# Kernel tuning notes

Hardware: AMD Instinct MI355X
Metric: run time of the kernel (lower is better)

Reference implementation:

```python
import jax, jax.numpy as jnp
import numpy as np

B, M, N, DQ, H = 4, 4096, 4096, 256, 64

def setup_inputs() -> dict:
    key = jax.random.key(0)
    k1, k2, k3, k4 = jax.random.split(key, 4)
    x = jax.random.normal(k1, (B, M, DQ), dtype=jnp.float32)
    cond = jax.random.normal(k2, (B, N, DQ), dtype=jnp.float32)
    Wq = jax.random.normal(k3, (DQ, H), dtype=jnp.float32) * (1.0 / np.sqrt(DQ))
    Wkv = jax.random.normal(k4, (DQ, 2 * H), dtype=jnp.float32) * (1.0 / np.sqrt(DQ))
    return {"x": x, "cond": cond, "Wq": Wq, "Wkv": Wkv}

def reference(x, cond, Wq, Wkv):
    h = Wq.shape[1]
    q = jnp.einsum('bmi,ih->bmh', x, Wq)          # [B,M,H]
    kv = jnp.einsum('bni,ih->bnh', cond, Wkv)     # [B,N,2H]
    k, v = jnp.split(kv, 2, axis=-1)              # each [B,N,H]
    qk = jnp.einsum('bmd,bnd->bmn', q, k) / jnp.sqrt(jnp.asarray(h, q.dtype))
    attn = jax.nn.softmax(qk, axis=-1)            # [B,M,N]
    out = jnp.einsum('bmn,bnd->bmd', attn, v)     # [B,M,H]
    return out
```

## Files before the change

### kernel.cpp

```cpp
#include <hip/hip_runtime.h>
#include <hip/hip_bf16.h>
#include <cstdint>


#define BB 4
#define MM 4096
#define NN 4096
#define DQm 256
#define DH 64
#define NSP 8
#define NITER (NN / 64 / NSP)
#define QSCALE 0.18033688011112042f

typedef _Float16 half8 __attribute__((ext_vector_type(8)));
typedef _Float16 half4 __attribute__((ext_vector_type(4)));
typedef float floatx16 __attribute__((ext_vector_type(16)));

static __device__ __forceinline__ unsigned pkrtz(float a, float b) {
    union { __fp16 h __attribute__((ext_vector_type(2))); unsigned u; } cv;
    cv.h = __builtin_amdgcn_cvt_pkrtz(a, b);
    return cv.u;
}

__global__ __launch_bounds__(256) void wtrans_kernel(const float* __restrict__ Wq,
                                                     const float* __restrict__ Wkv,
                                                     _Float16* __restrict__ wt) {
    int cout = blockIdx.x;
    int t = threadIdx.x;
    float v = (cout < 64) ? Wq[t * 64 + cout] * QSCALE : Wkv[t * 128 + (cout - 64)];
    _Float16 hi = (_Float16)v;
    _Float16 lo = (_Float16)(v - (float)hi);
    wt[cout * DQm + t] = hi;
    wt[192 * DQm + cout * DQm + t] = lo;
}

__global__ __launch_bounds__(256) void proj_kernel(const float* __restrict__ x,
                                                   const float* __restrict__ cond,
                                                   const _Float16* __restrict__ wt,
                                                   _Float16* __restrict__ q_h,
                                                   _Float16* __restrict__ k_h,
                                                   _Float16* __restrict__ vt_h) {
    __shared__ __align__(16) _Float16 xh[64][264];
    __shared__ __align__(16) _Float16 xl[64][264];
    const int t = threadIdx.x;
    const bool isq = blockIdx.x < (BB * MM / 64);
    const int blk = isq ? blockIdx.x : blockIdx.x - BB * MM / 64;
    const long row0 = (long)blk * 64;
    const float4* xg = (const float4*)((isq ? x : cond) + row0 * DQm);
#pragma unroll
    for (int it = 0; it < 16; ++it) {
        int fid = t + it * 256;
        int row = fid >> 6, c4 = fid & 63;
        float4 v = xg[fid];
        half4 hh = {(_Float16)v.x, (_Float16)v.y, (_Float16)v.z, (_Float16)v.w};
        half4 hl = {(_Float16)(v.x - (float)hh[0]), (_Float16)(v.y - (float)hh[1]),
                    (_Float16)(v.z - (float)hh[2]), (_Float16)(v.w - (float)hh[3])};
        *(half4*)(&xh[row][c4 * 4]) = hh;
        *(half4*)(&xl[row][c4 * 4]) = hl;
    }
    __syncthreads();
    const int lane = t & 63, w = t >> 6, c = lane & 31, h = lane >> 5;
    const _Float16* wlo = wt + 192 * DQm;

    if (isq) {
        const int rt = w & 1, ct = w >> 1;
        floatx16 a1, a2, a3;
#pragma unroll
        for (int i = 0; i < 16; ++i) { a1[i] = 0.f; a2[i] = 0.f; a3[i] = 0.f; }
#pragma unroll
        for (int kt = 0; kt < 16; ++kt) {
            half8 ah = *(const half8*)(&xh[rt * 32 + c][kt * 16 + h * 8]);
            half8 al = *(const half8*)(&xl[rt * 32 + c][kt * 16 + h * 8]);
            half8 bh = *(const half8*)(wt  + (long)(ct * 32 + c) * DQm + kt * 16 + h * 8);
            half8 bl = *(const half8*)(wlo + (long)(ct * 32 + c) * DQm + kt * 16 + h * 8);
            a1 = __builtin_amdgcn_mfma_f32_32x32x16_f16(ah, bh, a1, 0, 0, 0);
            a2 = __builtin_amdgcn_mfma_f32_32x32x16_f16(ah, bl, a2, 0, 0, 0);
            a3 = __builtin_amdgcn_mfma_f32_32x32x16_f16(al, bh, a3, 0, 0, 0);
        }
#pragma unroll
        for (int r = 0; r < 16; ++r) {
            int m = (r & 3) + 8 * (r >> 2) + 4 * h;
            q_h[(row0 + rt * 32 + m) * DH + ct * 32 + c] = (_Float16)(a1[r] + a2[r] + a3[r]);
        }
    } else {
        const int rt = w & 1, ctp = w >> 1;
        floatx16 a1[2], a2[2], a3[2];
#pragma unroll
        for (int i = 0; i < 16; ++i) {
            a1[0][i] = 0.f; a2[0][i] = 0.f; a3[0][i] = 0.f;
            a1[1][i] = 0.f; a2[1][i] = 0.f; a3[1][i] = 0.f;
        }
#pragma unroll
        for (int kt = 0; kt < 16; ++kt) {
            half8 ah = *(const half8*)(&xh[rt * 32 + c][kt * 16 + h * 8]);
            half8 al = *(const half8*)(&xl[rt * 32 + c][kt * 16 + h * 8]);
#pragma unroll
            for (int i = 0; i < 2; ++i) {
                long wrow = 64 + (ctp * 2 + i) * 32 + c;
                half8 bh = *(const half8*)(wt  + wrow * DQm + kt * 16 + h * 8);
                half8 bl = *(const half8*)(wlo + wrow * DQm + kt * 16 + h * 8);
                a1[i] = __builtin_amdgcn_mfma_f32_32x32x16_f16(ah, bh, a1[i], 0, 0, 0);
                a2[i] = __builtin_amdgcn_mfma_f32_32x32x16_f16(ah, bl, a2[i], 0, 0, 0);
                a3[i] = __builtin_amdgcn_mfma_f32_32x32x16_f16(al, bh, a3[i], 0, 0, 0);
            }
        }
#pragma unroll
        for (int i = 0; i < 2; ++i) {
            int cout = (ctp * 2 + i) * 32 + c;
            if (cout < 64) {
#pragma unroll
                for (int r = 0; r < 16; ++r) {
                    int m = (r & 3) + 8 * (r >> 2) + 4 * h;
                    k_h[(row0 + rt * 32 + m) * DH + cout] =
                        (_Float16)(a1[i][r] + a2[i][r] + a3[i][r]);
                }
            } else {
                int d = cout - 64;
                long bb = row0 >> 12;
#pragma unroll
                for (int s2 = 0; s2 < 4; ++s2) {
                    long n = row0 + rt * 32 + 8 * s2 + 4 * h;
                    half4 hv;
#pragma unroll
                    for (int j = 0; j < 4; ++j)
                        hv[j] = (_Float16)(a1[i][s2 * 4 + j] + a2[i][s2 * 4 + j] +
                                           a3[i][s2 * 4 + j]);
                    *(half4*)(vt_h + (bb * DH + d) * NN + (n & 4095)) = hv;
                }
            }
        }
    }
}

__global__ __launch_bounds__(256, 4) void fa_kernel(const _Float16* __restrict__ q_h,
                                                    const _Float16* __restrict__ k_h,
                                                    const _Float16* __restrict__ vt_h,
                                                    float* __restrict__ Opart,
                                                    float2* __restrict__ ml) {
    __shared__ __align__(16) _Float16 k_lds[64][72];
    __shared__ __align__(16) _Float16 vt_lds[64][72];

    const int t = threadIdx.x;
    const int w = t >> 6;
    const int lane = t & 63;
    const int c = lane & 31;
    const int h = lane >> 5;

    const int bid = blockIdx.x;
    const int sp = bid >> 7;
    const int b  = (bid >> 5) & 3;
    const int mt = bid & 31;
    const int mbase = mt * 128 + w * 32;
    const long qrow = (long)b * MM + mbase + c;

    half8 qf[4];
#pragma unroll
    for (int kt = 0; kt < 4; ++kt)
        qf[kt] = *(const half8*)(q_h + qrow * DH + kt * 16 + h * 8);

    floatx16 Oc0, Oc1;
#pragma unroll
    for (int i = 0; i < 16; ++i) { Oc0[i] = 0.f; Oc1[i] = 0.f; }
    float m_run = -INFINITY, l_run = 0.f;

#pragma unroll 1
    for (int nt = sp * NITER; nt < sp * NITER + NITER; ++nt) {
        const int n0 = nt * 64;
        __syncthreads();
        {
            const uint4* kg = (const uint4*)(k_h + ((long)b * NN + n0) * DH);
#pragma unroll
            for (int it = 0; it < 2; ++it) {
                int cid = t + it * 256;
                int r = cid >> 3, q = cid & 7;
                *(uint4*)(&k_lds[r][q * 8]) = kg[cid];
                *(uint4*)(&vt_lds[r][q * 8]) =
                    *(const uint4*)(vt_h + ((long)b * DH + r) * NN + n0 + q * 8);
            }
        }
        __syncthreads();

        floatx16 Sc[2];
#pragma unroll
        for (int a = 0; a < 2; ++a) {
            floatx16 acc;
#pragma unroll
            for (int i = 0; i < 16; ++i) acc[i] = 0.f;
#pragma unroll
            for (int kt = 0; kt < 4; ++kt) {
                half8 af = *(const half8*)(&k_lds[a * 32 + c][kt * 16 + h * 8]);
                acc = __builtin_amdgcn_mfma_f32_32x32x16_f16(af, qf[kt], acc, 0, 0, 0);
            }
            Sc[a] = acc;
        }

        float tmax = -INFINITY;
#pragma unroll
        for (int a = 0; a < 2; ++a)
#pragma unroll
            for (int r = 0; r < 16; ++r) tmax = fmaxf(tmax, Sc[a][r]);
        tmax = fmaxf(tmax, __shfl_xor(tmax, 32, 64));
        if (__any(tmax > m_run + 8.0f)) {
            float m_new = fmaxf(m_run, tmax);
            float alpha = exp2f(m_run - m_new);
            l_run *= alpha;
#pragma unroll
            for (int i = 0; i < 16; ++i) { Oc0[i] *= alpha; Oc1[i] *= alpha; }
            m_run = m_new;
        }
        float tsum = 0.f;
#pragma unroll
        for (int a = 0; a < 2; ++a)
#pragma unroll
            for (int r = 0; r < 16; ++r) {
                float p = exp2f(Sc[a][r] - m_run);
                Sc[a][r] = p;
                tsum += p;
            }
        tsum += __shfl_xor(tsum, 32, 64);
        l_run += tsum;

#pragma unroll
        for (int a = 0; a < 2; ++a) {
            uint2 pk0 = {pkrtz(Sc[a][0],  Sc[a][1]),  pkrtz(Sc[a][2],  Sc[a][3])};
            uint2 pk1 = {pkrtz(Sc[a][4],  Sc[a][5]),  pkrtz(Sc[a][6],  Sc[a][7])};
            uint2 pk2 = {pkrtz(Sc[a][8],  Sc[a][9]),  pkrtz(Sc[a][10], Sc[a][11])};
            uint2 pk3 = {pkrtz(Sc[a][12], Sc[a][13]), pkrtz(Sc[a][14], Sc[a][15])};
            union { uint4 u; half8 f; } f0, f1;
#if __has_builtin(__builtin_amdgcn_permlane32_swap)
            {
                auto r0 = __builtin_amdgcn_permlane32_swap(pk0.x, pk1.x, false, false);
                auto r1 = __builtin_amdgcn_permlane32_swap(pk0.y, pk1.y, false, false);
                auto r2 = __builtin_amdgcn_permlane32_swap(pk2.x, pk3.x, false, false);
                auto r3 = __builtin_amdgcn_permlane32_swap(pk2.y, pk3.y, false, false);
                f0.u.x = r0[0]; f0.u.z = r0[1];
                f0.u.y = r1[0]; f0.u.w = r1[1];
                f1.u.x = r2[0]; f1.u.z = r2[1];
                f1.u.y = r3[0]; f1.u.w = r3[1];
            }
#else
            {
                uint2 s0, s1, ex0, ex1;
                s0.x = h ? pk0.x : pk1.x;  s0.y = h ? pk0.y : pk1.y;
                s1.x = h ? pk2.x : pk3.x;  s1.y = h ? pk2.y : pk3.y;
                ex0.x = __shfl_xor((int)s0.x, 32, 64);
                ex0.y = __shfl_xor((int)s0.y, 32, 64);
                ex1.x = __shfl_xor((int)s1.x, 32, 64);
                ex1.y = __shfl_xor((int)s1.y, 32, 64);
                f0.u.x = h ? ex0.x : pk0.x;  f0.u.y = h ? ex0.y : pk0.y;
                f0.u.z = h ? pk1.x : ex0.x;  f0.u.w = h ? pk1.y : ex0.y;
                f1.u.x = h ? ex1.x : pk2.x;  f1.u.y = h ? ex1.y : pk2.y;
                f1.u.z = h ? pk3.x : ex1.x;  f1.u.w = h ? pk3.y : ex1.y;
            }
#endif
#pragma unroll
            for (int bq = 0; bq < 2; ++bq) {
                int kt = 2 * a + bq;
                half8 pf = bq ? f1.f : f0.f;
                half8 vf0 = *(const half8*)(&vt_lds[c][kt * 16 + h * 8]);
                half8 vf1 = *(const half8*)(&vt_lds[32 + c][kt * 16 + h * 8]);
                Oc0 = __builtin_amdgcn_mfma_f32_32x32x16_f16(vf0, pf, Oc0, 0, 0, 0);
                Oc1 = __builtin_amdgcn_mfma_f32_32x32x16_f16(vf1, pf, Oc1, 0, 0, 0);
            }
        }
    }

    const long obase = ((long)sp * BB * MM + (long)b * MM + mbase + c) * DH;
#pragma unroll
    for (int dt = 0; dt < 2; ++dt) {
        const floatx16& O = dt ? Oc1 : Oc0;
#pragma unroll
        for (int s2 = 0; s2 < 4; ++s2) {
            float4 v;
            v.x = O[s2 * 4 + 0]; v.y = O[s2 * 4 + 1];
            v.z = O[s2 * 4 + 2]; v.w = O[s2 * 4 + 3];
            *(float4*)(Opart + obase + dt * 32 + s2 * 8 + h * 4) = v;
        }
    }
    if (h == 0)
        ml[((long)sp * BB + b) * MM + mbase + c] = make_float2(m_run, l_run);
}

__global__ __launch_bounds__(256) void merge_kernel(const float* __restrict__ Opart,
                                                    const float2* __restrict__ ml,
                                                    float* __restrict__ out) {
    const long gid = (long)blockIdx.x * 256 + threadIdx.x;
    const long row = gid >> 6;
    float2 p[NSP];
    float mmax = -INFINITY;
#pragma unroll
    for (int i = 0; i < NSP; ++i) {
        p[i] = ml[(long)i * BB * MM + row];
        mmax = fmaxf(mmax, p[i].x);
    }
    float denom = 0.f, o = 0.f;
#pragma unroll
    for (int i = 0; i < NSP; ++i) {
        float ai = exp2f(p[i].x - mmax);
        denom += ai * p[i].y;
        o += ai * Opart[(long)i * BB * MM * DH + gid];
    }
    out[gid] = o / denom;
}

extern "C" void kernel_launch(void* const* d_in, const int* in_sizes, int n_in,
                              void* d_out, int out_size, void* d_ws, size_t ws_size,
                              hipStream_t stream) {
    const float* x    = (const float*)d_in[0];
    const float* cond = (const float*)d_in[1];
    const float* Wq   = (const float*)d_in[2];
    const float* Wkv  = (const float*)d_in[3];
    float* out = (float*)d_out;

    char* ws = (char*)d_ws;
    _Float16* wt   = (_Float16*)(ws);
    _Float16* q_h  = (_Float16*)(ws + 196608);
    _Float16* k_h  = (_Float16*)(ws + 196608 + 2097152);
    _Float16* vt_h = (_Float16*)(ws + 196608 + 2 * 2097152);
    float*    Op   = (float*)(ws + 196608 + 3 * 2097152);
    float2*   mlp  = (float2*)(ws + 196608 + 3 * 2097152 + (size_t)NSP * 4194304);

    wtrans_kernel<<<192, 256, 0, stream>>>(Wq, Wkv, wt);
    proj_kernel<<<BB * (MM + NN) / 64, 256, 0, stream>>>(x, cond, wt, q_h, k_h, vt_h);
    fa_kernel<<<NSP * BB * 32, 256, 0, stream>>>(q_h, k_h, vt_h, Op, mlp);
    merge_kernel<<<BB * MM * DH / 256, 256, 0, stream>>>(Op, mlp, out);
}
```

Baseline: 134.9 us.

## Double-buffer K/V tiles, compute row sums via MFMA, vectorize merge

The flash-attention loop now keeps two LDS buffers. It prefetches the next K/V tile into registers while the current tile is computed, and needs only one barrier per iteration instead of two. Row sums of P are computed by an extra MFMA against a ones fragment instead of a VALU reduction with a cross-lane shuffle, and the tile max uses a tree reduction. The merge kernel handles four outputs per thread with float4 loads and stores. The cost is doubled LDS, extra prefetch registers that may hurt occupancy at 4 waves per SIMD, and an additional MFMA per P-V step.

```diff
diff --git a/kernel.cpp b/kernel.cpp
--- a/kernel.cpp
+++ b/kernel.cpp
@@ -137,8 +137,8 @@
                                                     const _Float16* __restrict__ vt_h,
                                                     float* __restrict__ Opart,
                                                     float2* __restrict__ ml) {
-    __shared__ __align__(16) _Float16 k_lds[64][72];
-    __shared__ __align__(16) _Float16 vt_lds[64][72];
+    __shared__ __align__(16) _Float16 k_lds[2][64][72];
+    __shared__ __align__(16) _Float16 vt_lds[2][64][72];
 
     const int t = threadIdx.x;
     const int w = t >> 6;
@@ -153,32 +153,52 @@
     const int mbase = mt * 128 + w * 32;
     const long qrow = (long)b * MM + mbase + c;
 
+    const int r0 = t >> 3, qq = t & 7;
+    const uint4* kg = (const uint4*)(k_h + (long)b * NN * DH);
+    const _Float16* vp0 = vt_h + ((long)b * DH + r0) * NN + qq * 8;
+    const _Float16* vp1 = vp0 + 32 * NN;
+
     half8 qf[4];
 #pragma unroll
     for (int kt = 0; kt < 4; ++kt)
         qf[kt] = *(const half8*)(q_h + qrow * DH + kt * 16 + h * 8);
 
-    floatx16 Oc0, Oc1;
-#pragma unroll
-    for (int i = 0; i < 16; ++i) { Oc0[i] = 0.f; Oc1[i] = 0.f; }
-    float m_run = -INFINITY, l_run = 0.f;
+    half8 ones_frag;
+    {
+        const _Float16 ov = (c == 0 || c == 4) ? (_Float16)1.0f : (_Float16)0.0f;
+#pragma unroll
+        for (int j = 0; j < 8; ++j) ones_frag[j] = ov;
+    }
+
+    floatx16 Oc0, Oc1, Lc;
+#pragma unroll
+    for (int i = 0; i < 16; ++i) { Oc0[i] = 0.f; Oc1[i] = 0.f; Lc[i] = 0.f; }
+    float m_run = -INFINITY;
+
+    uint4 sk0, sk1, sv0, sv1;
+    {
+        const int n0 = sp * NITER * 64;
+        sk0 = kg[n0 * 8 + t];
+        sk1 = kg[n0 * 8 + t + 256];
+        sv0 = *(const uint4*)(vp0 + n0);
+        sv1 = *(const uint4*)(vp1 + n0);
+        *(uint4*)(&k_lds[0][r0][qq * 8]) = sk0;
+        *(uint4*)(&k_lds[0][r0 + 32][qq * 8]) = sk1;
+        *(uint4*)(&vt_lds[0][r0][qq * 8]) = sv0;
+        *(uint4*)(&vt_lds[0][r0 + 32][qq * 8]) = sv1;
+    }
+    __syncthreads();
 
 #pragma unroll 1
-    for (int nt = sp * NITER; nt < sp * NITER + NITER; ++nt) {
-        const int n0 = nt * 64;
-        __syncthreads();
-        {
-            const uint4* kg = (const uint4*)(k_h + ((long)b * NN + n0) * DH);
-#pragma unroll
-            for (int it = 0; it < 2; ++it) {
-                int cid = t + it * 256;
-                int r = cid >> 3, q = cid & 7;
-                *(uint4*)(&k_lds[r][q * 8]) = kg[cid];
-                *(uint4*)(&vt_lds[r][q * 8]) =
-                    *(const uint4*)(vt_h + ((long)b * DH + r) * NN + n0 + q * 8);
-            }
-        }
-        __syncthreads();
+    for (int it = 0; it < NITER; ++it) {
+        const int pb = it & 1;
+        if (it + 1 < NITER) {
+            const int n0 = (sp * NITER + it + 1) * 64;
+            sk0 = kg[n0 * 8 + t];
+            sk1 = kg[n0 * 8 + t + 256];
+            sv0 = *(const uint4*)(vp0 + n0);
+            sv1 = *(const uint4*)(vp1 + n0);
+        }
 
         floatx16 Sc[2];
 #pragma unroll
@@ -188,37 +208,33 @@
             for (int i = 0; i < 16; ++i) acc[i] = 0.f;
 #pragma unroll
             for (int kt = 0; kt < 4; ++kt) {
-                half8 af = *(const half8*)(&k_lds[a * 32 + c][kt * 16 + h * 8]);
+                half8 af = *(const half8*)(&k_lds[pb][a * 32 + c][kt * 16 + h * 8]);
                 acc = __builtin_amdgcn_mfma_f32_32x32x16_f16(af, qf[kt], acc, 0, 0, 0);
             }
             Sc[a] = acc;
         }
 
-        float tmax = -INFINITY;
-#pragma unroll
-        for (int a = 0; a < 2; ++a)
-#pragma unroll
-            for (int r = 0; r < 16; ++r) tmax = fmaxf(tmax, Sc[a][r]);
+        float t8[8];
+#pragma unroll
+        for (int i = 0; i < 8; ++i)
+            t8[i] = fmaxf(fmaxf(Sc[0][2 * i], Sc[0][2 * i + 1]),
+                          fmaxf(Sc[1][2 * i], Sc[1][2 * i + 1]));
+        float ta = fmaxf(fmaxf(t8[0], t8[1]), t8[2]);
+        float tb = fmaxf(fmaxf(t8[3], t8[4]), t8[5]);
+        float tmax = fmaxf(fmaxf(ta, tb), fmaxf(t8[6], t8[7]));
         tmax = fmaxf(tmax, __shfl_xor(tmax, 32, 64));
         if (__any(tmax > m_run + 8.0f)) {
             float m_new = fmaxf(m_run, tmax);
             float alpha = exp2f(m_run - m_new);
-            l_run *= alpha;
 #pragma unroll
             for (int i = 0; i < 16; ++i) { Oc0[i] *= alpha; Oc1[i] *= alpha; }
+            Lc[0] *= alpha;
             m_run = m_new;
         }
-        float tsum = 0.f;
 #pragma unroll
         for (int a = 0; a < 2; ++a)
 #pragma unroll
-            for (int r = 0; r < 16; ++r) {
-                float p = exp2f(Sc[a][r] - m_run);
-                Sc[a][r] = p;
-                tsum += p;
-            }
-        tsum += __shfl_xor(tsum, 32, 64);
-        l_run += tsum;
+            for (int r = 0; r < 16; ++r) Sc[a][r] = exp2f(Sc[a][r] - m_run);
 
 #pragma unroll
         for (int a = 0; a < 2; ++a) {
@@ -229,14 +245,14 @@
             union { uint4 u; half8 f; } f0, f1;
 #if __has_builtin(__builtin_amdgcn_permlane32_swap)
             {
-                auto r0 = __builtin_amdgcn_permlane32_swap(pk0.x, pk1.x, false, false);
-                auto r1 = __builtin_amdgcn_permlane32_swap(pk0.y, pk1.y, false, false);
-                auto r2 = __builtin_amdgcn_permlane32_swap(pk2.x, pk3.x, false, false);
-                auto r3 = __builtin_amdgcn_permlane32_swap(pk2.y, pk3.y, false, false);
-                f0.u.x = r0[0]; f0.u.z = r0[1];
-                f0.u.y = r1[0]; f0.u.w = r1[1];
-                f1.u.x = r2[0]; f1.u.z = r2[1];
-                f1.u.y = r3[0]; f1.u.w = r3[1];
+                auto r0s = __builtin_amdgcn_permlane32_swap(pk0.x, pk1.x, false, false);
+                auto r1s = __builtin_amdgcn_permlane32_swap(pk0.y, pk1.y, false, false);
+                auto r2s = __builtin_amdgcn_permlane32_swap(pk2.x, pk3.x, false, false);
+                auto r3s = __builtin_amdgcn_permlane32_swap(pk2.y, pk3.y, false, false);
+                f0.u.x = r0s[0]; f0.u.z = r0s[1];
+                f0.u.y = r1s[0]; f0.u.w = r1s[1];
+                f1.u.x = r2s[0]; f1.u.z = r2s[1];
+                f1.u.y = r3s[0]; f1.u.w = r3s[1];
             }
 #else
             {
@@ -257,11 +273,21 @@
             for (int bq = 0; bq < 2; ++bq) {
                 int kt = 2 * a + bq;
                 half8 pf = bq ? f1.f : f0.f;
-                half8 vf0 = *(const half8*)(&vt_lds[c][kt * 16 + h * 8]);
-                half8 vf1 = *(const half8*)(&vt_lds[32 + c][kt * 16 + h * 8]);
+                half8 vf0 = *(const half8*)(&vt_lds[pb][c][kt * 16 + h * 8]);
+                half8 vf1 = *(const half8*)(&vt_lds[pb][32 + c][kt * 16 + h * 8]);
                 Oc0 = __builtin_amdgcn_mfma_f32_32x32x16_f16(vf0, pf, Oc0, 0, 0, 0);
                 Oc1 = __builtin_amdgcn_mfma_f32_32x32x16_f16(vf1, pf, Oc1, 0, 0, 0);
-            }
+                Lc  = __builtin_amdgcn_mfma_f32_32x32x16_f16(ones_frag, pf, Lc, 0, 0, 0);
+            }
+        }
+
+        if (it + 1 < NITER) {
+            const int pn = pb ^ 1;
+            *(uint4*)(&k_lds[pn][r0][qq * 8]) = sk0;
+            *(uint4*)(&k_lds[pn][r0 + 32][qq * 8]) = sk1;
+            *(uint4*)(&vt_lds[pn][r0][qq * 8]) = sv0;
+            *(uint4*)(&vt_lds[pn][r0 + 32][qq * 8]) = sv1;
+            __syncthreads();
         }
     }
 
@@ -278,14 +304,14 @@
         }
     }
     if (h == 0)
-        ml[((long)sp * BB + b) * MM + mbase + c] = make_float2(m_run, l_run);
+        ml[((long)sp * BB + b) * MM + mbase + c] = make_float2(m_run, Lc[0]);
 }
 
 __global__ __launch_bounds__(256) void merge_kernel(const float* __restrict__ Opart,
                                                     const float2* __restrict__ ml,
                                                     float* __restrict__ out) {
-    const long gid = (long)blockIdx.x * 256 + threadIdx.x;
-    const long row = gid >> 6;
+    const long g4 = (long)blockIdx.x * 256 + threadIdx.x;
+    const long row = g4 >> 4;
     float2 p[NSP];
     float mmax = -INFINITY;
 #pragma unroll
@@ -293,14 +319,19 @@
         p[i] = ml[(long)i * BB * MM + row];
         mmax = fmaxf(mmax, p[i].x);
     }
-    float denom = 0.f, o = 0.f;
+    float denom = 0.f;
+    float4 o = make_float4(0.f, 0.f, 0.f, 0.f);
+    const float4* Op4 = (const float4*)Opart;
 #pragma unroll
     for (int i = 0; i < NSP; ++i) {
         float ai = exp2f(p[i].x - mmax);
         denom += ai * p[i].y;
-        o += ai * Opart[(long)i * BB * MM * DH + gid];
-    }
-    out[gid] = o / denom;
+        float4 v = Op4[(long)i * (BB * MM * DH / 4) + g4];
+        o.x += ai * v.x; o.y += ai * v.y; o.z += ai * v.z; o.w += ai * v.w;
+    }
+    float inv = 1.0f / denom;
+    o.x *= inv; o.y *= inv; o.z *= inv; o.w *= inv;
+    ((float4*)out)[g4] = o;
 }
 
 extern "C" void kernel_launch(void* const* d_in, const int* in_sizes, int n_in,
@@ -323,5 +354,5 @@
     wtrans_kernel<<<192, 256, 0, stream>>>(Wq, Wkv, wt);
     proj_kernel<<<BB * (MM + NN) / 64, 256, 0, stream>>>(x, cond, wt, q_h, k_h, vt_h);
     fa_kernel<<<NSP * BB * 32, 256, 0, stream>>>(q_h, k_h, vt_h, Op, mlp);
-    merge_kernel<<<BB * MM * DH / 256, 256, 0, stream>>>(Op, mlp, out);
-}
+    merge_kernel<<<BB * MM * DH / 4 / 256, 256, 0, stream>>>(Op, mlp, out);
+}
```

Result: slower. 143.0 us (+6.0%).
